# Kernel tuning notes

Measured on AMD Instinct MI355X. Metric: run time of the kernel, lower is better.

The kernel has to match this reference:

```python
import jax, jax.numpy as jnp
import numpy as np
from jax import lax

L = 25            # max_delay (250 // init_spike_step=10, odd)
SIG = 12.0        # max_delay // 2, frozen (requires_grad=False)
BN_EPS = 1e-5
EPS = 1e-7


def _dcls_kernel(W, P):
    # Gaussian interpolation of kernel_count=1 weights onto a dense kernel of size L.
    # W, P: (out, in). Returns (out, in, L).
    grid = jnp.arange(L, dtype=W.dtype) - L // 2          # (L,)
    K = jnp.exp(-0.5 * ((grid[None, None, :] - P[:, :, None]) / SIG) ** 2)
    K = K / (jnp.sum(K, axis=-1, keepdims=True) + EPS)    # normalize over kernel taps
    return W[:, :, None] * K


def _dcls_conv(x_tbc, W, P):
    # x_tbc: (T, B, Cin) -> causal dilated-kernel conv over time -> (T, B, Cout)
    kernel = _dcls_kernel(W, P)                           # (Cout, Cin, L)
    xb = jnp.transpose(x_tbc, (1, 2, 0))                  # (B, Cin, T)
    xb = jnp.pad(xb, ((0, 0), (0, 0), (L - 1, 0)))        # left (causal) padding
    y = lax.conv_general_dilated(xb, kernel, window_strides=(1,), padding='VALID',
                                 dimension_numbers=('NCH', 'OIH', 'NCH'))
    return jnp.transpose(y, (2, 0, 1))                    # (T, B, Cout)


def _bn(x_tbc, gamma, beta):
    # BatchNorm1d with step_mode='m': stats over merged (T, B) per channel.
    mean = jnp.mean(x_tbc, axis=(0, 1))
    var = jnp.var(x_tbc, axis=(0, 1))
    xhat = (x_tbc - mean) * lax.rsqrt(var + BN_EPS)
    return gamma * xhat + beta


def setup_inputs() -> dict:
    key = jax.random.key(0)
    ks = jax.random.split(key, 8)
    B, T, C = 128, 100, 700
    x = jax.random.uniform(ks[0], (B, T, C), dtype=jnp.float32)
    pmax = float(L // 2)
    W1 = jax.random.normal(ks[1], (256, 700), jnp.float32) * (1.0 / np.sqrt(700))
    P1 = jax.random.uniform(ks[2], (256, 700), jnp.float32, minval=-pmax, maxval=pmax)
    W2 = jax.random.normal(ks[3], (256, 256), jnp.float32) * (1.0 / np.sqrt(256))
    P2 = jax.random.uniform(ks[4], (256, 256), jnp.float32, minval=-pmax, maxval=pmax)
    W3 = jax.random.normal(ks[5], (20, 256), jnp.float32) * (1.0 / np.sqrt(256))
    P3 = jax.random.uniform(ks[6], (20, 256), jnp.float32, minval=-pmax, maxval=pmax)
    return {
        'x': x, 'W1': W1, 'P1': P1, 'W2': W2, 'P2': P2, 'W3': W3, 'P3': P3,
        'gamma1': jnp.ones((256,), jnp.float32), 'beta1': jnp.zeros((256,), jnp.float32),
        'gamma2': jnp.ones((256,), jnp.float32), 'beta2': jnp.zeros((256,), jnp.float32),
    }


def reference(x, W1, P1, W2, P2, W3, P3, gamma1, beta1, gamma2, beta2):
    h = jnp.transpose(x, (1, 0, 2))            # (T, B, C)
    h = _dcls_conv(h, W1, P1)                  # (T, B, 256)
    h = jax.nn.relu(_bn(h, gamma1, beta1))     # dropout = identity (eval)
    h = _dcls_conv(h, W2, P2)                  # (T, B, 256)
    h = jax.nn.relu(_bn(h, gamma2, beta2))
    h = _dcls_conv(h, W3, P3)                  # (T, B, 20)
    return jnp.sum(jax.nn.softmax(h, axis=2), axis=0)   # (B, 20)
```

## Files before the change

### kernel.cpp

```cpp
#include <hip/hip_runtime.h>
#include <stdint.h>


#define T_LEN 100
#define B_SZ  128
#define M_ROWS 12800
#define R_RANK 4
#define K_FIR 448

typedef __bf16 v8bf __attribute__((ext_vector_type(8)));
typedef float  v4f  __attribute__((ext_vector_type(4)));
typedef unsigned int uint32;
typedef unsigned short ushort_t;

struct PhiT { float v[25][R_RANK]; };
constexpr double cexp_(double x) {
  double s = 1.0, t = 1.0;
  for (int n = 1; n < 30; ++n) { t = t * x / n; s += t; }
  return s;
}
constexpr PhiT make_phi() {
  PhiT P{};
  for (int tau = 0; tau < 25; ++tau) {
    double u = (tau - 12) / 12.0;
    double g = cexp_(-0.5 * u * u);
    double T0 = 1.0, T1 = u;
    P.v[tau][0] = (float)(g * T0);
    P.v[tau][1] = (float)(g * T1);
    for (int r = 2; r < R_RANK; ++r) {
      double T2 = 2.0 * u * T1 - T0;
      P.v[tau][r] = (float)(g * T2);
      T0 = T1; T1 = T2;
    }
  }
  return P;
}
constexpr PhiT PHI = make_phi();

__device__ __forceinline__ void gl_lds16(const void* g, void* l) {
  __builtin_amdgcn_global_load_lds(
      (const __attribute__((address_space(1))) char*)g,
      (__attribute__((address_space(3))) char*)l, 16, 0, 0);
}

__device__ __forceinline__ void build_wr_body(
    const float* __restrict__ W, const float* __restrict__ P,
    __bf16* __restrict__ Wr, int CIN, int CINP, int COUT, int COUTP, int o) {
  for (int i = threadIdx.x; i < CINP; i += blockDim.x) {
    bool valid = (o < COUT) && (i < CIN);
    float w = valid ? W[(size_t)o * CIN + i] : 0.f;
    float p = valid ? P[(size_t)o * CIN + i] : 0.f;
    float S = 0.f;
#pragma unroll
    for (int l = 0; l < 25; ++l) {
      float d = ((float)(l - 12) - p) * (1.f / 12.f);
      S += expf(-0.5f * d * d);
    }
    float v = p * (1.f / 12.f);
    float g = w * expf(-0.5f * v * v) / (S + 1e-7f);
    float h = 0.5f * v, hh = h * h;
    float pw = 1.f;
#pragma unroll
    for (int r = 0; r < R_RANK; ++r) {
      float term = pw, sum = pw;
#pragma unroll
      for (int m = 1; m <= 6; ++m) {
        term *= hh / (float)(m * (m + r));
        sum += term;
      }
      float c = g * ((r == 0) ? 1.f : 2.f) * sum;
      Wr[((size_t)r * COUTP + o) * CINP + i] = (__bf16)c;
      pw *= h / (float)(r + 1);
    }
  }
}

__global__ void setup_all(const float* __restrict__ x,
                          const float* __restrict__ W1, const float* __restrict__ P1,
                          const float* __restrict__ W2, const float* __restrict__ P2,
                          const float* __restrict__ W3, const float* __restrict__ P3,
                          __bf16* __restrict__ Xb, __bf16* __restrict__ Wr1,
                          __bf16* __restrict__ Wr2, __bf16* __restrict__ Wr3,
                          __bf16* __restrict__ Af, float* __restrict__ stats) {
  int blk = blockIdx.x;
  if (blk < 256) { build_wr_body(W1, P1, Wr1, 700, 704, 256, 256, blk); return; }
  blk -= 256;
  if (blk < 256) { build_wr_body(W2, P2, Wr2, 256, 256, 256, 256, blk); return; }
  blk -= 256;
  if (blk < 32) { build_wr_body(W3, P3, Wr3, 256, 256, 20, 32, blk); return; }
  blk -= 32;
  if (blk < 196) {
    int idx = blk * 256 + threadIdx.x;
    if (idx < 112 * 448) {
      int t = idx / 448, k = idx - t * 448;
      float v = 0.f;
      if (t < 100 && k < 400) {
        int r = k / 100, s = k - r * 100;
        int tau = s - t + 24;
        if (tau >= 0 && tau < 25) v = PHI.v[tau][r];
      }
      Af[idx] = (__bf16)v;
    }
    return;
  }
  blk -= 196;
  if (blk < 12800) {
    int t = blk >> 7, b = blk & 127;
    const float* src = x + ((size_t)b * T_LEN + t) * 700;
    __bf16* dst = Xb + (size_t)blk * 704;
    for (int c = threadIdx.x; c < 704; c += 256) dst[c] = (c < 700) ? (__bf16)src[c] : (__bf16)0.f;
    return;
  }
  blk -= 12800;
  if (blk == 0) {
    for (int i = threadIdx.x; i < 1024; i += 256) stats[i] = 0.f;
  }
}

template <int CINP, int BLK_N, int WROWS, int WCOLS, int CO_SH>
__global__ __launch_bounds__(256, 2)
void gemm_rk64(const __bf16* __restrict__ A, const __bf16* __restrict__ Bm,
               __bf16* __restrict__ Z) {
  constexpr int COUTP = 1 << CO_SH;
  constexpr int WM = 128 / WROWS;
  constexpr int WN = BLK_N / WCOLS;
  constexpr int RM = WM / 16;
  constexpr int RN = WN / 16;
  __shared__ __align__(16) __bf16 sA[128 * 64];
  __shared__ __align__(16) __bf16 sB[BLK_N * 64];

  const int tid = threadIdx.x;
  const int w = tid >> 6, lane = tid & 63;
  const int q = lane >> 4, ln = lane & 15;
  const int wrow = w / WCOLS, wcol = w % WCOLS;
  const int srow8 = lane >> 3;
  const int s8 = lane & 7;

  const int t0 = blockIdx.x;
  const int oc = blockIdx.y * BLK_N;
  const __bf16* Abase = A + (size_t)t0 * 128 * CINP;
  const __bf16* Bbase = Bm + (size_t)oc * CINP;

  v4f acc[RM][RN];
#pragma unroll
  for (int a = 0; a < RM; ++a)
#pragma unroll
    for (int b = 0; b < RN; ++b) acc[a][b] = v4f{0.f, 0.f, 0.f, 0.f};

  for (int ic = 0; ic < CINP; ic += 64) {
    for (int j = w; j < 16; j += 4) {
      int m = j * 8 + srow8;
      int g = s8 ^ (m & 7);
      gl_lds16(Abase + (size_t)m * CINP + ic + g * 8, &sA[j * 512]);
    }
    for (int j = w; j < BLK_N / 8; j += 4) {
      int n = j * 8 + srow8;
      int g = s8 ^ (n & 7);
      gl_lds16(Bbase + (size_t)n * CINP + ic + g * 8, &sB[j * 512]);
    }
    __syncthreads();

#pragma unroll
    for (int s = 0; s < 2; ++s) {
      v8bf af[RM], bfr[RN];
#pragma unroll
      for (int a = 0; a < RM; ++a) {
        int m = wrow * WM + a * 16 + ln;
        af[a] = *(const v8bf*)&sA[m * 64 + ((((s << 2) | q) ^ (m & 7)) * 8)];
      }
#pragma unroll
      for (int b = 0; b < RN; ++b) {
        int n = wcol * WN + b * 16 + ln;
        bfr[b] = *(const v8bf*)&sB[n * 64 + ((((s << 2) | q) ^ (n & 7)) * 8)];
      }
#pragma unroll
      for (int a = 0; a < RM; ++a)
#pragma unroll
        for (int b = 0; b < RN; ++b)
          acc[a][b] = __builtin_amdgcn_mfma_f32_16x16x32_bf16(af[a], bfr[b], acc[a][b], 0, 0, 0);
    }
    __syncthreads();
  }

#pragma unroll
  for (int a = 0; a < RM; ++a) {
#pragma unroll
    for (int b = 0; b < RN; ++b) {
      int n = oc + wcol * WN + b * 16 + ln;
      int r = n >> CO_SH, o = n & (COUTP - 1);
#pragma unroll
      for (int rr = 0; rr < 4; ++rr) {
        int m = t0 * 128 + wrow * WM + a * 16 + q * 4 + rr;
        Z[((size_t)r * M_ROWS + m) * COUTP + o] = (__bf16)acc[a][b][rr];
      }
    }
  }
}

template <int COUTP, bool STATS, bool SOFTMAX>
__global__ __launch_bounds__(256, 2)
void fir_gemm64(const __bf16* __restrict__ Af, const __bf16* __restrict__ Z,
                __bf16* __restrict__ Yout, float* __restrict__ stats,
                float* __restrict__ outp, int N) {
  __shared__ __align__(16) unsigned char smem[26624];
  __bf16* sA = (__bf16*)smem;
  uint32* sBu = (uint32*)(smem + 14336);

  const int tid = threadIdx.x;
  const int w = tid >> 6, lane = tid & 63;
  const int q = lane >> 4, ln = lane & 15;
  const int srow8 = lane >> 3, s8 = lane & 7;
  const int kp = tid >> 3;
  const int noct = tid & 7;
  const int nb = blockIdx.x * 64;

  v4f acc[7];
#pragma unroll
  for (int a = 0; a < 7; ++a) acc[a] = v4f{0.f, 0.f, 0.f, 0.f};

  for (int kc = 0; kc < K_FIR; kc += 64) {
    for (int j = w; j < 14; j += 4) {
      int m = j * 8 + srow8;
      int g = s8 ^ (m & 7);
      gl_lds16(Af + (size_t)m * K_FIR + kc + g * 8, &sA[j * 512]);
    }
    const __bf16* zp = Z + (size_t)(kc + kp * 2) * N + nb + noct * 8;
    uint4 r0 = *(const uint4*)zp;
    uint4 r1 = *(const uint4*)(zp + N);
    const ushort_t* p0 = (const ushort_t*)&r0;
    const ushort_t* p1 = (const ushort_t*)&r1;
#pragma unroll
    for (int j = 0; j < 8; ++j) {
      uint32 val = (uint32)p0[j] | ((uint32)p1[j] << 16);
      sBu[(noct * 8 + j) * 35 + kp] = val;
    }
    __syncthreads();

#pragma unroll
    for (int s = 0; s < 2; ++s) {
      v8bf af[7];
#pragma unroll
      for (int a = 0; a < 7; ++a) {
        int m = a * 16 + ln;
        af[a] = *(const v8bf*)&sA[m * 64 + ((((s << 2) | q) ^ (m & 7)) * 8)];
      }
      int base = (w * 16 + ln) * 35 + s * 16 + q * 4;
      uint32 tmp[4] = {sBu[base], sBu[base + 1], sBu[base + 2], sBu[base + 3]};
      v8bf bfr = *(const v8bf*)tmp;
#pragma unroll
      for (int a = 0; a < 7; ++a)
        acc[a] = __builtin_amdgcn_mfma_f32_16x16x32_bf16(af[a], bfr, acc[a], 0, 0, 0);
    }
    __syncthreads();
  }

  int ng = nb + w * 16 + ln;
  if (!SOFTMAX) {
    float s = 0.f, ss = 0.f;
#pragma unroll
    for (int a = 0; a < 7; ++a) {
#pragma unroll
      for (int rr = 0; rr < 4; ++rr) {
        int t = a * 16 + q * 4 + rr;
        float v = acc[a][rr];
        if (t < 100) {
          Yout[(size_t)t * N + ng] = (__bf16)v;
          s += v; ss += v * v;
        }
      }
    }
    if (STATS) {
      s += __shfl_xor(s, 16); ss += __shfl_xor(ss, 16);
      s += __shfl_xor(s, 32); ss += __shfl_xor(ss, 32);
      if (q == 0) {
        int o = ng & (COUTP - 1);
        atomicAdd(&stats[o], s);
        atomicAdd(&stats[COUTP + o], ss);
      }
    }
  } else {
    float* smx = (float*)smem;
    float* lacc = (float*)(smem + 26000);
    int col = w * 16 + ln;
#pragma unroll
    for (int a = 0; a < 7; ++a) {
#pragma unroll
      for (int rr = 0; rr < 4; ++rr) {
        int t = a * 16 + q * 4 + rr;
        if (t < 100) smx[t * 65 + col] = acc[a][rr];
      }
    }
    if (tid < 64) lacc[tid & 63] = 0.f;
    __syncthreads();
    if (tid < 200) {
      int bl = tid / 100, t = tid - bl * 100;
      const float* rr = &smx[t * 65 + bl * 32];
      float v[20], m = -1e30f;
#pragma unroll
      for (int o = 0; o < 20; ++o) { v[o] = rr[o]; m = fmaxf(m, v[o]); }
      float sum = 0.f;
#pragma unroll
      for (int o = 0; o < 20; ++o) { v[o] = expf(v[o] - m); sum += v[o]; }
      float inv = 1.f / sum;
#pragma unroll
      for (int o = 0; o < 20; ++o) atomicAdd(&lacc[bl * 20 + o], v[o] * inv);
    }
    __syncthreads();
    if (tid < 40) {
      int bl = tid / 20, o = tid - bl * 20;
      int b = (nb >> 5) + bl;
      outp[b * 20 + o] = lacc[bl * 20 + o];
    }
  }
}

__global__ __launch_bounds__(256)
void bn_apply_relu8(__bf16* __restrict__ h, const float* __restrict__ stats,
                    const float* __restrict__ gamma, const float* __restrict__ beta) {
  int idx = blockIdx.x * 256 + threadIdx.x;
  int co = (idx & 31) * 8;
  size_t row = (size_t)(idx >> 5);
  __bf16* p = h + row * 256 + co;
  uint4 raw = *(const uint4*)p;
  const ushort_t* pr = (const ushort_t*)&raw;
  uint4 outv;
  ushort_t* po = (ushort_t*)&outv;
#pragma unroll
  for (int j = 0; j < 8; ++j) {
    int c = co + j;
    float mean = stats[c] * (1.f / 12800.f);
    float var = stats[256 + c] * (1.f / 12800.f) - mean * mean;
    float inv = rsqrtf(var + 1e-5f) * gamma[c];
    uint32 u = (uint32)pr[j] << 16;
    float xv; __builtin_memcpy(&xv, &u, 4);
    float v = (xv - mean) * inv + beta[c];
    v = fmaxf(v, 0.f);
    __bf16 bv = (__bf16)v;
    po[j] = *(const ushort_t*)&bv;
  }
  *(uint4*)p = outv;
}


extern "C" void kernel_launch(void* const* d_in, const int* in_sizes, int n_in,
                              void* d_out, int out_size, void* d_ws, size_t ws_size,
                              hipStream_t stream) {
  const float* x  = (const float*)d_in[0];
  const float* W1 = (const float*)d_in[1];
  const float* P1 = (const float*)d_in[2];
  const float* W2 = (const float*)d_in[3];
  const float* P2 = (const float*)d_in[4];
  const float* W3 = (const float*)d_in[5];
  const float* P3 = (const float*)d_in[6];
  const float* g1 = (const float*)d_in[7];
  const float* b1 = (const float*)d_in[8];
  const float* g2 = (const float*)d_in[9];
  const float* b2 = (const float*)d_in[10];
  float* out = (float*)d_out;

  constexpr size_t XB_B  = (size_t)M_ROWS * 704 * 2;
  constexpr size_t Z_B   = (size_t)K_FIR * 32768 * 2;
  constexpr size_t Y12_B = (size_t)M_ROWS * 256 * 2;
  constexpr size_t W1_B  = (size_t)R_RANK * 256 * 704 * 2;
  constexpr size_t W2_B  = (size_t)R_RANK * 256 * 256 * 2;
  constexpr size_t W3_B  = (size_t)R_RANK * 32 * 256 * 2;
  constexpr size_t AF_B  = (size_t)112 * K_FIR * 2;
  constexpr size_t ST_B  = 4096;
  constexpr size_t TOTAL = XB_B + Z_B + Y12_B + W1_B + W2_B + W3_B + AF_B + ST_B;
  if (ws_size < TOTAL) return;

  char* ws = (char*)d_ws;
  size_t off = 0;
  __bf16* Xb   = (__bf16*)(ws + off); off += XB_B;
  __bf16* Zb   = (__bf16*)(ws + off); off += Z_B;
  __bf16* Yb   = (__bf16*)(ws + off); off += Y12_B;
  __bf16* Wr1  = (__bf16*)(ws + off); off += W1_B;
  __bf16* Wr2  = (__bf16*)(ws + off); off += W2_B;
  __bf16* Wr3  = (__bf16*)(ws + off); off += W3_B;
  __bf16* Afir = (__bf16*)(ws + off); off += AF_B;
  float*  stats1 = (float*)(ws + off);
  float*  stats2 = stats1 + 512;

  setup_all<<<dim3(13541), 256, 0, stream>>>(x, W1, P1, W2, P2, W3, P3,
                                             Xb, Wr1, Wr2, Wr3, Afir, stats1);

  gemm_rk64<704, 256, 2, 2, 8><<<dim3(100, 4), 256, 0, stream>>>(Xb, Wr1, Zb);
  fir_gemm64<256, true, false><<<dim3(512), 256, 0, stream>>>(
      Afir, Zb, Yb, stats1, nullptr, 32768);
  bn_apply_relu8<<<dim3(1600), 256, 0, stream>>>(Yb, stats1, g1, b1);

  gemm_rk64<256, 256, 2, 2, 8><<<dim3(100, 4), 256, 0, stream>>>(Yb, Wr2, Zb);
  fir_gemm64<256, true, false><<<dim3(512), 256, 0, stream>>>(
      Afir, Zb, Yb, stats2, nullptr, 32768);
  bn_apply_relu8<<<dim3(1600), 256, 0, stream>>>(Yb, stats2, g2, b2);

  gemm_rk64<256, 64, 2, 2, 5><<<dim3(100, 2), 256, 0, stream>>>(Yb, Wr3, Zb);
  fir_gemm64<32, false, true><<<dim3(64), 256, 0, stream>>>(
      Afir, Zb, nullptr, nullptr, out, 4096);
}
```

Baseline: 198.7 us.

## Fuse BatchNorm apply and ReLU into FIR GEMM via grid-wide barrier

Removes the separate bn_apply_relu8 kernels. Each FIR GEMM block now accumulates channel statistics, signals a global semaphore, spins until all 512 blocks arrive, then normalizes and applies ReLU on its in-register results before writing bf16 once. This saves a kernel launch plus a full read/write pass over the 12800x256 activation per layer. In exchange it relies on all 512 blocks being co-resident, which launch bounds of 2 blocks per CU on 256 CUs should allow, and adds spin-wait cost; otherwise the kernel deadlocks.

```diff
diff --git a/kernel.cpp b/kernel.cpp
--- a/kernel.cpp
+++ b/kernel.cpp
@@ -113,7 +113,7 @@
   }
   blk -= 12800;
   if (blk == 0) {
-    for (int i = threadIdx.x; i < 1024; i += 256) stats[i] = 0.f;
+    for (int i = threadIdx.x; i < 1088; i += 256) stats[i] = 0.f;
   }
 }
 
@@ -201,7 +201,9 @@
 __global__ __launch_bounds__(256, 2)
 void fir_gemm64(const __bf16* __restrict__ Af, const __bf16* __restrict__ Z,
                 __bf16* __restrict__ Yout, float* __restrict__ stats,
-                float* __restrict__ outp, int N) {
+                float* __restrict__ outp, int N,
+                const float* __restrict__ gamma, const float* __restrict__ beta,
+                uint32* __restrict__ sem, int nblk) {
   __shared__ __align__(16) unsigned char smem[26624];
   __bf16* sA = (__bf16*)smem;
   uint32* sBu = (uint32*)(smem + 14336);
@@ -263,19 +265,39 @@
       for (int rr = 0; rr < 4; ++rr) {
         int t = a * 16 + q * 4 + rr;
         float v = acc[a][rr];
+        if (t < 100) { s += v; ss += v * v; }
+      }
+    }
+    s += __shfl_xor(s, 16); ss += __shfl_xor(ss, 16);
+    s += __shfl_xor(s, 32); ss += __shfl_xor(ss, 32);
+    int o = ng & (COUTP - 1);
+    if (q == 0) {
+      atomicAdd(&stats[o], s);
+      atomicAdd(&stats[COUTP + o], ss);
+    }
+    __threadfence();
+    __syncthreads();
+    if (tid == 0) {
+      __hip_atomic_fetch_add(sem, 1u, __ATOMIC_RELEASE, __HIP_MEMORY_SCOPE_AGENT);
+      while (__hip_atomic_load(sem, __ATOMIC_ACQUIRE, __HIP_MEMORY_SCOPE_AGENT) < (uint32)nblk)
+        __builtin_amdgcn_s_sleep(2);
+    }
+    __syncthreads();
+    float sum  = __hip_atomic_load(&stats[o], __ATOMIC_RELAXED, __HIP_MEMORY_SCOPE_AGENT);
+    float ssum = __hip_atomic_load(&stats[COUTP + o], __ATOMIC_RELAXED, __HIP_MEMORY_SCOPE_AGENT);
+    float mean = sum * (1.f / 12800.f);
+    float var  = ssum * (1.f / 12800.f) - mean * mean;
+    float inv  = rsqrtf(var + 1e-5f) * gamma[o];
+    float bet  = beta[o];
+#pragma unroll
+    for (int a = 0; a < 7; ++a) {
+#pragma unroll
+      for (int rr = 0; rr < 4; ++rr) {
+        int t = a * 16 + q * 4 + rr;
         if (t < 100) {
+          float v = fmaxf((acc[a][rr] - mean) * inv + bet, 0.f);
           Yout[(size_t)t * N + ng] = (__bf16)v;
-          s += v; ss += v * v;
         }
-      }
-    }
-    if (STATS) {
-      s += __shfl_xor(s, 16); ss += __shfl_xor(ss, 16);
-      s += __shfl_xor(s, 32); ss += __shfl_xor(ss, 32);
-      if (q == 0) {
-        int o = ng & (COUTP - 1);
-        atomicAdd(&stats[o], s);
-        atomicAdd(&stats[COUTP + o], ss);
       }
     }
   } else {
@@ -312,33 +334,6 @@
       outp[b * 20 + o] = lacc[bl * 20 + o];
     }
   }
-}
-
-__global__ __launch_bounds__(256)
-void bn_apply_relu8(__bf16* __restrict__ h, const float* __restrict__ stats,
-                    const float* __restrict__ gamma, const float* __restrict__ beta) {
-  int idx = blockIdx.x * 256 + threadIdx.x;
-  int co = (idx & 31) * 8;
-  size_t row = (size_t)(idx >> 5);
-  __bf16* p = h + row * 256 + co;
-  uint4 raw = *(const uint4*)p;
-  const ushort_t* pr = (const ushort_t*)&raw;
-  uint4 outv;
-  ushort_t* po = (ushort_t*)&outv;
-#pragma unroll
-  for (int j = 0; j < 8; ++j) {
-    int c = co + j;
-    float mean = stats[c] * (1.f / 12800.f);
-    float var = stats[256 + c] * (1.f / 12800.f) - mean * mean;
-    float inv = rsqrtf(var + 1e-5f) * gamma[c];
-    uint32 u = (uint32)pr[j] << 16;
-    float xv; __builtin_memcpy(&xv, &u, 4);
-    float v = (xv - mean) * inv + beta[c];
-    v = fmaxf(v, 0.f);
-    __bf16 bv = (__bf16)v;
-    po[j] = *(const ushort_t*)&bv;
-  }
-  *(uint4*)p = outv;
 }
 
 
@@ -365,7 +360,7 @@
   constexpr size_t W2_B  = (size_t)R_RANK * 256 * 256 * 2;
   constexpr size_t W3_B  = (size_t)R_RANK * 32 * 256 * 2;
   constexpr size_t AF_B  = (size_t)112 * K_FIR * 2;
-  constexpr size_t ST_B  = 4096;
+  constexpr size_t ST_B  = 8192;
   constexpr size_t TOTAL = XB_B + Z_B + Y12_B + W1_B + W2_B + W3_B + AF_B + ST_B;
   if (ws_size < TOTAL) return;
 
@@ -380,21 +375,21 @@
   __bf16* Afir = (__bf16*)(ws + off); off += AF_B;
   float*  stats1 = (float*)(ws + off);
   float*  stats2 = stats1 + 512;
+  uint32* sem1   = (uint32*)(stats1 + 1024);
+  uint32* sem2   = sem1 + 1;
 
   setup_all<<<dim3(13541), 256, 0, stream>>>(x, W1, P1, W2, P2, W3, P3,
                                              Xb, Wr1, Wr2, Wr3, Afir, stats1);
 
   gemm_rk64<704, 256, 2, 2, 8><<<dim3(100, 4), 256, 0, stream>>>(Xb, Wr1, Zb);
   fir_gemm64<256, true, false><<<dim3(512), 256, 0, stream>>>(
-      Afir, Zb, Yb, stats1, nullptr, 32768);
-  bn_apply_relu8<<<dim3(1600), 256, 0, stream>>>(Yb, stats1, g1, b1);
+      Afir, Zb, Yb, stats1, nullptr, 32768, g1, b1, sem1, 512);
 
   gemm_rk64<256, 256, 2, 2, 8><<<dim3(100, 4), 256, 0, stream>>>(Yb, Wr2, Zb);
   fir_gemm64<256, true, false><<<dim3(512), 256, 0, stream>>>(
-      Afir, Zb, Yb, stats2, nullptr, 32768);
-  bn_apply_relu8<<<dim3(1600), 256, 0, stream>>>(Yb, stats2, g2, b2);
+      Afir, Zb, Yb, stats2, nullptr, 32768, g2, b2, sem2, 512);
 
   gemm_rk64<256, 64, 2, 2, 5><<<dim3(100, 2), 256, 0, stream>>>(Yb, Wr3, Zb);
   fir_gemm64<32, false, true><<<dim3(64), 256, 0, stream>>>(
-      Afir, Zb, nullptr, nullptr, out, 4096);
-}
+      Afir, Zb, nullptr, nullptr, out, 4096, nullptr, nullptr, nullptr, 0);
+}
```

Measured after the change: 309.6 us. 1.56x slower.

## Double-buffer FIR GEMM shared tiles and vectorize input bf16 conversion

Applied to the files above, without the earlier changes.

The FIR GEMM kernel now double-buffers its shared-memory A and B tiles, issuing the next chunk's global loads before computing on the current one, so load latency can overlap MFMA work. Barriers and explicit waitcnt replace the two syncthreads per iteration. Separately, the x-to-bf16 conversion in setup uses float4 loads and packed 8-byte stores over far fewer blocks. Shared memory per block nearly doubles, which may limit occupancy, and the LDS write of one buffer's B tile overlaps reads of the other buffer under custom synchronization.

```diff
diff --git a/kernel.cpp b/kernel.cpp
--- a/kernel.cpp
+++ b/kernel.cpp
@@ -104,14 +104,28 @@
     return;
   }
   blk -= 196;
-  if (blk < 12800) {
-    int t = blk >> 7, b = blk & 127;
-    const float* src = x + ((size_t)b * T_LEN + t) * 700;
-    __bf16* dst = Xb + (size_t)blk * 704;
-    for (int c = threadIdx.x; c < 704; c += 256) dst[c] = (c < 700) ? (__bf16)src[c] : (__bf16)0.f;
+  if (blk < 2200) {
+    int c0 = blk * 1024 + threadIdx.x;
+#pragma unroll
+    for (int k = 0; k < 4; ++k) {
+      int c = c0 + k * 256;
+      int row = c / 176, col4 = c - row * 176;
+      int t = row >> 7, b = row & 127;
+      uint2 pk;
+      __bf16* pb = (__bf16*)&pk;
+      if (col4 < 175) {
+        const float* src = x + ((size_t)b * T_LEN + t) * 700 + col4 * 4;
+        float4 v = *(const float4*)src;
+        pb[0] = (__bf16)v.x; pb[1] = (__bf16)v.y;
+        pb[2] = (__bf16)v.z; pb[3] = (__bf16)v.w;
+      } else {
+        pk.x = 0u; pk.y = 0u;
+      }
+      *(uint2*)&Xb[(size_t)row * 704 + col4 * 4] = pk;
+    }
     return;
   }
-  blk -= 12800;
+  blk -= 2200;
   if (blk == 0) {
     for (int i = threadIdx.x; i < 1024; i += 256) stats[i] = 0.f;
   }
@@ -202,9 +216,7 @@
 void fir_gemm64(const __bf16* __restrict__ Af, const __bf16* __restrict__ Z,
                 __bf16* __restrict__ Yout, float* __restrict__ stats,
                 float* __restrict__ outp, int N) {
-  __shared__ __align__(16) unsigned char smem[26624];
-  __bf16* sA = (__bf16*)smem;
-  uint32* sBu = (uint32*)(smem + 14336);
+  __shared__ __align__(16) unsigned char smem[46592];
 
   const int tid = threadIdx.x;
   const int w = tid >> 6, lane = tid & 63;
@@ -218,40 +230,71 @@
 #pragma unroll
   for (int a = 0; a < 7; ++a) acc[a] = v4f{0.f, 0.f, 0.f, 0.f};
 
-  for (int kc = 0; kc < K_FIR; kc += 64) {
+  uint4 r0, r1;
+
+#define SA_BUF(b) ((__bf16*)(smem + (b) * 23296))
+#define SB_BUF(b) ((uint32*)(smem + (b) * 23296 + 14336))
+
+  {
+    __bf16* sA = SA_BUF(0);
     for (int j = w; j < 14; j += 4) {
       int m = j * 8 + srow8;
       int g = s8 ^ (m & 7);
-      gl_lds16(Af + (size_t)m * K_FIR + kc + g * 8, &sA[j * 512]);
-    }
-    const __bf16* zp = Z + (size_t)(kc + kp * 2) * N + nb + noct * 8;
-    uint4 r0 = *(const uint4*)zp;
-    uint4 r1 = *(const uint4*)(zp + N);
-    const ushort_t* p0 = (const ushort_t*)&r0;
-    const ushort_t* p1 = (const ushort_t*)&r1;
-#pragma unroll
-    for (int j = 0; j < 8; ++j) {
-      uint32 val = (uint32)p0[j] | ((uint32)p1[j] << 16);
-      sBu[(noct * 8 + j) * 35 + kp] = val;
-    }
-    __syncthreads();
-
-#pragma unroll
-    for (int s = 0; s < 2; ++s) {
-      v8bf af[7];
-#pragma unroll
-      for (int a = 0; a < 7; ++a) {
-        int m = a * 16 + ln;
-        af[a] = *(const v8bf*)&sA[m * 64 + ((((s << 2) | q) ^ (m & 7)) * 8)];
-      }
-      int base = (w * 16 + ln) * 35 + s * 16 + q * 4;
-      uint32 tmp[4] = {sBu[base], sBu[base + 1], sBu[base + 2], sBu[base + 3]};
-      v8bf bfr = *(const v8bf*)tmp;
-#pragma unroll
-      for (int a = 0; a < 7; ++a)
-        acc[a] = __builtin_amdgcn_mfma_f32_16x16x32_bf16(af[a], bfr, acc[a], 0, 0, 0);
-    }
-    __syncthreads();
+      gl_lds16(Af + (size_t)m * K_FIR + 0 + g * 8, &sA[j * 512]);
+    }
+    const __bf16* zp = Z + (size_t)(0 + kp * 2) * N + nb + noct * 8;
+    r0 = *(const uint4*)zp;
+    r1 = *(const uint4*)(zp + N);
+  }
+
+  for (int i = 0; i < 7; ++i) {
+    const int cb = i & 1;
+    asm volatile("s_waitcnt vmcnt(0)" ::: "memory");
+    {
+      uint32* sBu = SB_BUF(cb);
+      const ushort_t* p0 = (const ushort_t*)&r0;
+      const ushort_t* p1 = (const ushort_t*)&r1;
+#pragma unroll
+      for (int j = 0; j < 8; ++j) {
+        uint32 val = (uint32)p0[j] | ((uint32)p1[j] << 16);
+        sBu[(noct * 8 + j) * 35 + kp] = val;
+      }
+    }
+    if (i < 6) {
+      int kc = (i + 1) * 64;
+      __bf16* sA = SA_BUF(cb ^ 1);
+      for (int j = w; j < 14; j += 4) {
+        int m = j * 8 + srow8;
+        int g = s8 ^ (m & 7);
+        gl_lds16(Af + (size_t)m * K_FIR + kc + g * 8, &sA[j * 512]);
+      }
+      const __bf16* zp = Z + (size_t)(kc + kp * 2) * N + nb + noct * 8;
+      r0 = *(const uint4*)zp;
+      r1 = *(const uint4*)(zp + N);
+    }
+    asm volatile("s_waitcnt lgkmcnt(0)" ::: "memory");
+    __builtin_amdgcn_s_barrier();
+
+    {
+      __bf16* sA = SA_BUF(cb);
+      uint32* sBu = SB_BUF(cb);
+#pragma unroll
+      for (int s = 0; s < 2; ++s) {
+        v8bf af[7];
+#pragma unroll
+        for (int a = 0; a < 7; ++a) {
+          int m = a * 16 + ln;
+          af[a] = *(const v8bf*)&sA[m * 64 + ((((s << 2) | q) ^ (m & 7)) * 8)];
+        }
+        int base = (w * 16 + ln) * 35 + s * 16 + q * 4;
+        uint32 tmp[4] = {sBu[base], sBu[base + 1], sBu[base + 2], sBu[base + 3]};
+        v8bf bfr = *(const v8bf*)tmp;
+#pragma unroll
+        for (int a = 0; a < 7; ++a)
+          acc[a] = __builtin_amdgcn_mfma_f32_16x16x32_bf16(af[a], bfr, acc[a], 0, 0, 0);
+      }
+    }
+    __builtin_amdgcn_s_barrier();
   }
 
   int ng = nb + w * 16 + ln;
@@ -312,6 +355,8 @@
       outp[b * 20 + o] = lacc[bl * 20 + o];
     }
   }
+#undef SA_BUF
+#undef SB_BUF
 }
 
 __global__ __launch_bounds__(256)
@@ -381,8 +426,8 @@
   float*  stats1 = (float*)(ws + off);
   float*  stats2 = stats1 + 512;
 
-  setup_all<<<dim3(13541), 256, 0, stream>>>(x, W1, P1, W2, P2, W3, P3,
-                                             Xb, Wr1, Wr2, Wr3, Afir, stats1);
+  setup_all<<<dim3(2941), 256, 0, stream>>>(x, W1, P1, W2, P2, W3, P3,
+                                            Xb, Wr1, Wr2, Wr3, Afir, stats1);
 
   gemm_rk64<704, 256, 2, 2, 8><<<dim3(100, 4), 256, 0, stream>>>(Xb, Wr1, Zb);
   fir_gemm64<256, true, false><<<dim3(512), 256, 0, stream>>>(
```

After: 187.5 us, median of 2. 5.6% less time.
